# Kernel tuning notes

Hardware: AMD Instinct MI355X
Metric: run time of the kernel (lower is better)

## Reference

```python
import jax, jax.numpy as jnp
import numpy as np

MAX_VAL = 100000000.0

B, H, S, D = 4, 16, 2048, 64


def setup_inputs() -> dict:
    key = jax.random.key(0)
    kq, kk, kv, km = jax.random.split(key, 4)
    query = jax.random.normal(kq, (B, H, S, D), dtype=jnp.float32)
    key_t = jax.random.normal(kk, (B, H, S, D), dtype=jnp.float32)
    value = jax.random.normal(kv, (B, H, S, D), dtype=jnp.float32)
    mask = jax.random.randint(km, (B, 1, S, S), 0, 2, dtype=jnp.int32)
    return {"query": query, "key": key_t, "value": value, "mask": mask}


def reference(query, key, value, mask):
    d = query.shape[-1]
    # scores: [B, H, S, S]
    scores = jnp.einsum("bhqd,bhkd->bhqk", query, key) / jnp.sqrt(jnp.float32(d))
    scores = jnp.where(mask == 1, -MAX_VAL, scores)
    p_attn = jax.nn.softmax(scores, axis=-1)
    out = jnp.einsum("bhqk,bhkd->bhqd", p_attn, value)
    return out, p_attn
```

## Files before the change

kernel.cpp:

```cpp
#include <hip/hip_runtime.h>
#include <hip/hip_bf16.h>


#define SDIM 2048
#define DDIM 64
#define NB 4
#define NH 16
#define BHN 64
#define TQ 16
#define OUT_ELEMS (BHN * SDIM * DDIM)

typedef float f32x4 __attribute__((ext_vector_type(4)));
typedef __bf16 bf16x8 __attribute__((ext_vector_type(8)));
typedef __bf16 bf16x4 __attribute__((ext_vector_type(4)));
typedef __bf16 bf16;

__global__ void cvt_qk_kernel(const float* __restrict__ q, const float* __restrict__ k,
                              bf16* __restrict__ Qb, bf16* __restrict__ Kb,
                              int n8, float qscale) {
    int i = blockIdx.x * blockDim.x + threadIdx.x;
    const float* src;
    bf16* dst;
    float scale;
    if (i < n8) {
        src = q; dst = Qb; scale = qscale;
    } else {
        src = k; dst = Kb; scale = 1.0f; i -= n8;
    }
    const f32x4* s4 = (const f32x4*)src;
    f32x4 a = __builtin_nontemporal_load(s4 + 2 * i);
    f32x4 c = __builtin_nontemporal_load(s4 + 2 * i + 1);
    bf16x8 o;
    o[0] = (bf16)(a[0] * scale); o[1] = (bf16)(a[1] * scale);
    o[2] = (bf16)(a[2] * scale); o[3] = (bf16)(a[3] * scale);
    o[4] = (bf16)(c[0] * scale); o[5] = (bf16)(c[1] * scale);
    o[6] = (bf16)(c[2] * scale); o[7] = (bf16)(c[3] * scale);
    *(bf16x8*)(dst + 8 * (size_t)i) = o;
}

__global__ void transpose_v_kernel(const float* __restrict__ v, bf16* __restrict__ vt) {
    int bh = blockIdx.x >> 5;
    int k0 = (blockIdx.x & 31) * 64;
    __shared__ bf16 tile[64][72];
    int t = threadIdx.x;
    int r = t >> 4;
    int c4 = (t & 15) * 4;
    const float* vb = v + (size_t)bh * SDIM * DDIM;
#pragma unroll
    for (int i = 0; i < 4; i++) {
        int row = r + 16 * i;
        f32x4 x = __builtin_nontemporal_load(
            (const f32x4*)(vb + (size_t)(k0 + row) * DDIM + c4));
        tile[c4 + 0][row] = (bf16)x[0];
        tile[c4 + 1][row] = (bf16)x[1];
        tile[c4 + 2][row] = (bf16)x[2];
        tile[c4 + 3][row] = (bf16)x[3];
    }
    __syncthreads();
    bf16* vtb = vt + (size_t)bh * DDIM * SDIM;
    int drow = t >> 2;
    int seg = (t & 3) * 16;
    uint4 u0 = *(const uint4*)&tile[drow][seg];
    uint4 u1 = *(const uint4*)&tile[drow][seg + 8];
    *(uint4*)(vtb + (size_t)drow * SDIM + k0 + seg) = u0;
    *(uint4*)(vtb + (size_t)drow * SDIM + k0 + seg + 8) = u1;
}

__global__ void pack_mask_kernel(const int* __restrict__ src, unsigned* __restrict__ dst) {
    int i = blockIdx.x * blockDim.x + threadIdx.x;
    int mv = __builtin_nontemporal_load(src + i);
    unsigned long long bal = __ballot(mv == 1);
    int l = threadIdx.x & 63;
    if (l == 0) dst[i >> 5] = (unsigned)bal;
    else if (l == 32) dst[i >> 5] = (unsigned)(bal >> 32);
}

__launch_bounds__(256, 2)
__global__ void attn_kernel(const bf16* __restrict__ Qb, const bf16* __restrict__ Kb,
                            const bf16* __restrict__ Vtb, const unsigned* __restrict__ mbits,
                            float* __restrict__ out, float* __restrict__ p_out) {
    const int bid0 = blockIdx.x;
    const int bid = (bid0 & 7) * 1024 + (bid0 >> 3);
    const int qt = bid & 127;
    const int bh = bid >> 7;
    const int b  = bh >> 4;
    const int t = threadIdx.x;
    const int w = t >> 6;
    const int lane = t & 63;
    const int quad = lane >> 4;
    const int l15 = lane & 15;

    __shared__ bf16 pb[TQ * 2056];
    __shared__ float redmax[4][16];
    __shared__ float redsum[4][16];

    const int qrow = qt * TQ + l15;
    const bf16* qbase = Qb + ((size_t)bh * SDIM + qrow) * DDIM + 8 * quad;
    bf16x8 aq0 = *(const bf16x8*)(qbase);
    bf16x8 aq1 = *(const bf16x8*)(qbase + 32);

    const unsigned* mrow = mbits + (size_t)b * SDIM * 64
                         + (size_t)(qt * TQ + quad * 4) * 64 + w * 16;
    uint4 mw[4][4];
#pragma unroll
    for (int r = 0; r < 4; r++)
#pragma unroll
        for (int g = 0; g < 4; g++)
            mw[r][g] = *(const uint4*)(mrow + r * 64 + g * 4);

    f32x4 acc[32];
    const bf16* kbase = Kb + ((size_t)bh * SDIM + w * 512 + l15) * DDIM + 8 * quad;
#pragma unroll
    for (int kt = 0; kt < 32; kt++) {
        const bf16* kp = kbase + (size_t)kt * 16 * DDIM;
        bf16x8 b0 = *(const bf16x8*)(kp);
        bf16x8 b1 = *(const bf16x8*)(kp + 32);
        f32x4 c = {0.f, 0.f, 0.f, 0.f};
        c = __builtin_amdgcn_mfma_f32_16x16x32_bf16(aq0, b0, c, 0, 0, 0);
        c = __builtin_amdgcn_mfma_f32_16x16x32_bf16(aq1, b1, c, 0, 0, 0);
        acc[kt] = c;
    }

    const float MASKED = -1.4426950e8f;
    float mx[4] = {-3e38f, -3e38f, -3e38f, -3e38f};
#pragma unroll
    for (int kt = 0; kt < 32; kt++) {
        const int g = kt >> 3;
        const int sel = (kt >> 1) & 3;
#pragma unroll
        for (int r = 0; r < 4; r++) {
            const uint4 u = mw[r][g];
            unsigned dw = sel == 0 ? u.x : sel == 1 ? u.y : sel == 2 ? u.z : u.w;
            unsigned bits = dw >> (((kt & 1) << 4) + l15);
            float s = (bits & 1u) ? MASKED : acc[kt][r];
            acc[kt][r] = s;
            mx[r] = fmaxf(mx[r], s);
        }
    }
#pragma unroll
    for (int off = 1; off < 16; off <<= 1) {
#pragma unroll
        for (int r = 0; r < 4; r++)
            mx[r] = fmaxf(mx[r], __shfl_xor(mx[r], off, 64));
    }

    float sm[4] = {0.f, 0.f, 0.f, 0.f};
#pragma unroll
    for (int kt = 0; kt < 32; kt++) {
#pragma unroll
        for (int r = 0; r < 4; r++) {
            float e = __builtin_amdgcn_exp2f(acc[kt][r] - mx[r]);
            acc[kt][r] = e;
            sm[r] += e;
        }
    }
#pragma unroll
    for (int off = 1; off < 16; off <<= 1) {
#pragma unroll
        for (int r = 0; r < 4; r++)
            sm[r] += __shfl_xor(sm[r], off, 64);
    }

    if (l15 == 0) {
#pragma unroll
        for (int r = 0; r < 4; r++) {
            redmax[w][quad * 4 + r] = mx[r];
            redsum[w][quad * 4 + r] = sm[r];
        }
    }
    __syncthreads();
    float rs[4];
#pragma unroll
    for (int r = 0; r < 4; r++) {
        const int row = quad * 4 + r;
        float m0 = redmax[0][row], m1 = redmax[1][row];
        float m2 = redmax[2][row], m3 = redmax[3][row];
        float mg = fmaxf(fmaxf(m0, m1), fmaxf(m2, m3));
        float stot = redsum[0][row] * __builtin_amdgcn_exp2f(m0 - mg)
                   + redsum[1][row] * __builtin_amdgcn_exp2f(m1 - mg)
                   + redsum[2][row] * __builtin_amdgcn_exp2f(m2 - mg)
                   + redsum[3][row] * __builtin_amdgcn_exp2f(m3 - mg);
        rs[r] = __builtin_amdgcn_exp2f(mx[r] - mg) / stot;
    }

    const int j  = l15 & 3;
    const int c4 = l15 & 12;
    float* prow4 = p_out + (size_t)bh * SDIM * SDIM
                 + (size_t)(qt * TQ + quad * 4 + j) * SDIM + w * 512 + c4;
    bf16* pbrow = pb + (size_t)(quad * 4 + j) * 2056 + w * 512 + c4;
#pragma unroll
    for (int kt = 0; kt < 32; kt++) {
        float v0 = acc[kt][0] * rs[0];
        float v1 = acc[kt][1] * rs[1];
        float v2 = acc[kt][2] * rs[2];
        float v3 = acc[kt][3] * rs[3];
        float a  = (j & 1) ? v0 : v1;
        float bt = (j & 1) ? v2 : v3;
        a  = __shfl_xor(a, 1, 64);
        bt = __shfl_xor(bt, 1, 64);
        float nv0 = (j & 1) ? a  : v0;
        float nv1 = (j & 1) ? v1 : a;
        float nv2 = (j & 1) ? bt : v2;
        float nv3 = (j & 1) ? v3 : bt;
        a  = (j & 2) ? nv0 : nv2;
        bt = (j & 2) ? nv1 : nv3;
        a  = __shfl_xor(a, 2, 64);
        bt = __shfl_xor(bt, 2, 64);
        v0 = (j & 2) ? a   : nv0;
        v1 = (j & 2) ? bt  : nv1;
        v2 = (j & 2) ? nv2 : a;
        v3 = (j & 2) ? nv3 : bt;
        f32x4 pv = {v0, v1, v2, v3};
        __builtin_nontemporal_store(pv, (f32x4*)(prow4 + kt * 16));
        bf16x4 ph = {(bf16)v0, (bf16)v1, (bf16)v2, (bf16)v3};
        *(bf16x4*)(pbrow + kt * 16) = ph;
    }

    asm volatile("s_waitcnt lgkmcnt(0)" ::: "memory");
    __builtin_amdgcn_s_barrier();
    __builtin_amdgcn_sched_barrier(0);

    f32x4 o0 = {0.f, 0.f, 0.f, 0.f}, o1 = o0, o2 = o0, o3 = o0;
    const bf16* vbase = Vtb + ((size_t)bh * DDIM + w * 16 + l15) * SDIM + 8 * quad;
    const bf16* pbase = pb + l15 * 2056 + 8 * quad;
    __builtin_amdgcn_s_setprio(1);
#pragma unroll
    for (int ks = 0; ks < 64; ks += 4) {
        bf16x8 a0 = *(const bf16x8*)(pbase + 32 * ks);
        bf16x8 a1 = *(const bf16x8*)(pbase + 32 * (ks + 1));
        bf16x8 a2 = *(const bf16x8*)(pbase + 32 * (ks + 2));
        bf16x8 a3 = *(const bf16x8*)(pbase + 32 * (ks + 3));
        bf16x8 w0 = *(const bf16x8*)(vbase + 32 * ks);
        bf16x8 w1 = *(const bf16x8*)(vbase + 32 * (ks + 1));
        bf16x8 w2 = *(const bf16x8*)(vbase + 32 * (ks + 2));
        bf16x8 w3 = *(const bf16x8*)(vbase + 32 * (ks + 3));
        o0 = __builtin_amdgcn_mfma_f32_16x16x32_bf16(a0, w0, o0, 0, 0, 0);
        o1 = __builtin_amdgcn_mfma_f32_16x16x32_bf16(a1, w1, o1, 0, 0, 0);
        o2 = __builtin_amdgcn_mfma_f32_16x16x32_bf16(a2, w2, o2, 0, 0, 0);
        o3 = __builtin_amdgcn_mfma_f32_16x16x32_bf16(a3, w3, o3, 0, 0, 0);
    }
    __builtin_amdgcn_s_setprio(0);
    f32x4 o = (o0 + o1) + (o2 + o3);
    float* orow = out + ((size_t)bh * SDIM + qt * TQ + quad * 4) * DDIM + w * 16 + l15;
#pragma unroll
    for (int r = 0; r < 4; r++)
        __builtin_nontemporal_store(o[r], orow + (size_t)r * DDIM);
}

extern "C" void kernel_launch(void* const* d_in, const int* in_sizes, int n_in,
                              void* d_out, int out_size, void* d_ws, size_t ws_size,
                              hipStream_t stream) {
    const float* q = (const float*)d_in[0];
    const float* k = (const float*)d_in[1];
    const float* v = (const float*)d_in[2];
    const int* mask = (const int*)d_in[3];
    float* out = (float*)d_out;
    float* p = out + (size_t)OUT_ELEMS;

    bf16* Qb  = (bf16*)d_ws;
    bf16* Kb  = Qb + (size_t)BHN * SDIM * DDIM;
    bf16* Vtb = Kb + (size_t)BHN * SDIM * DDIM;
    unsigned* Mb = (unsigned*)(Vtb + (size_t)BHN * SDIM * DDIM);

    const float SC = 0.125f * 1.44269504f;
    cvt_qk_kernel<<<8192, 256, 0, stream>>>(q, k, Qb, Kb, OUT_ELEMS / 8, SC);
    transpose_v_kernel<<<BHN * (SDIM / 64), 256, 0, stream>>>(v, Vtb);
    pack_mask_kernel<<<(NB * SDIM * SDIM) / 256, 256, 0, stream>>>(mask, Mb);
    attn_kernel<<<BHN * (SDIM / TQ), 256, 0, stream>>>(Qb, Kb, Vtb, Mb, out, p);
}
```

Measured before the change: 1.599 ms.

## Split attention tile work across eight waves with LDS reduction of PV partials

Doubles the attention block to 512 threads so each wave handles 256 key columns instead of 512, halving per-thread score registers and mask words. The PV product is split into two key halves across wave pairs, and their partial outputs are combined through shared memory before storing. The aim is to raise occupancy and latency hiding on this memory-bound kernel, which writes the full P matrix. The cost is an extra barrier, more LDS, and a longer cross-wave max/sum reduction.

```diff
diff --git a/kernel.cpp b/kernel.cpp
--- a/kernel.cpp
+++ b/kernel.cpp
@@ -75,7 +75,7 @@
     else if (l == 32) dst[i >> 5] = (unsigned)(bal >> 32);
 }
 
-__launch_bounds__(256, 2)
+__launch_bounds__(512, 4)
 __global__ void attn_kernel(const bf16* __restrict__ Qb, const bf16* __restrict__ Kb,
                             const bf16* __restrict__ Vtb, const unsigned* __restrict__ mbits,
                             float* __restrict__ out, float* __restrict__ p_out) {
@@ -91,27 +91,19 @@
     const int l15 = lane & 15;
 
     __shared__ bf16 pb[TQ * 2056];
-    __shared__ float redmax[4][16];
-    __shared__ float redsum[4][16];
+    __shared__ float redmax[8][16];
+    __shared__ float redsum[8][16];
+    __shared__ f32x4 opart[4][64];
 
     const int qrow = qt * TQ + l15;
     const bf16* qbase = Qb + ((size_t)bh * SDIM + qrow) * DDIM + 8 * quad;
     bf16x8 aq0 = *(const bf16x8*)(qbase);
     bf16x8 aq1 = *(const bf16x8*)(qbase + 32);
 
-    const unsigned* mrow = mbits + (size_t)b * SDIM * 64
-                         + (size_t)(qt * TQ + quad * 4) * 64 + w * 16;
-    uint4 mw[4][4];
-#pragma unroll
-    for (int r = 0; r < 4; r++)
-#pragma unroll
-        for (int g = 0; g < 4; g++)
-            mw[r][g] = *(const uint4*)(mrow + r * 64 + g * 4);
-
-    f32x4 acc[32];
-    const bf16* kbase = Kb + ((size_t)bh * SDIM + w * 512 + l15) * DDIM + 8 * quad;
-#pragma unroll
-    for (int kt = 0; kt < 32; kt++) {
+    f32x4 acc[16];
+    const bf16* kbase = Kb + ((size_t)bh * SDIM + w * 256 + l15) * DDIM + 8 * quad;
+#pragma unroll
+    for (int kt = 0; kt < 16; kt++) {
         const bf16* kp = kbase + (size_t)kt * 16 * DDIM;
         bf16x8 b0 = *(const bf16x8*)(kp);
         bf16x8 b1 = *(const bf16x8*)(kp + 32);
@@ -121,10 +113,19 @@
         acc[kt] = c;
     }
 
+    const unsigned* mrow = mbits + (size_t)b * SDIM * 64
+                         + (size_t)(qt * TQ + quad * 4) * 64 + w * 8;
+    uint4 mw[4][2];
+#pragma unroll
+    for (int r = 0; r < 4; r++)
+#pragma unroll
+        for (int g = 0; g < 2; g++)
+            mw[r][g] = *(const uint4*)(mrow + r * 64 + g * 4);
+
     const float MASKED = -1.4426950e8f;
     float mx[4] = {-3e38f, -3e38f, -3e38f, -3e38f};
 #pragma unroll
-    for (int kt = 0; kt < 32; kt++) {
+    for (int kt = 0; kt < 16; kt++) {
         const int g = kt >> 3;
         const int sel = (kt >> 1) & 3;
 #pragma unroll
@@ -146,7 +147,7 @@
 
     float sm[4] = {0.f, 0.f, 0.f, 0.f};
 #pragma unroll
-    for (int kt = 0; kt < 32; kt++) {
+    for (int kt = 0; kt < 16; kt++) {
 #pragma unroll
         for (int r = 0; r < 4; r++) {
             float e = __builtin_amdgcn_exp2f(acc[kt][r] - mx[r]);
@@ -173,23 +174,27 @@
 #pragma unroll
     for (int r = 0; r < 4; r++) {
         const int row = quad * 4 + r;
-        float m0 = redmax[0][row], m1 = redmax[1][row];
-        float m2 = redmax[2][row], m3 = redmax[3][row];
-        float mg = fmaxf(fmaxf(m0, m1), fmaxf(m2, m3));
-        float stot = redsum[0][row] * __builtin_amdgcn_exp2f(m0 - mg)
-                   + redsum[1][row] * __builtin_amdgcn_exp2f(m1 - mg)
-                   + redsum[2][row] * __builtin_amdgcn_exp2f(m2 - mg)
-                   + redsum[3][row] * __builtin_amdgcn_exp2f(m3 - mg);
+        float mv[8];
+        float mg = -3e38f;
+#pragma unroll
+        for (int ww = 0; ww < 8; ww++) {
+            mv[ww] = redmax[ww][row];
+            mg = fmaxf(mg, mv[ww]);
+        }
+        float stot = 0.f;
+#pragma unroll
+        for (int ww = 0; ww < 8; ww++)
+            stot += redsum[ww][row] * __builtin_amdgcn_exp2f(mv[ww] - mg);
         rs[r] = __builtin_amdgcn_exp2f(mx[r] - mg) / stot;
     }
 
     const int j  = l15 & 3;
     const int c4 = l15 & 12;
     float* prow4 = p_out + (size_t)bh * SDIM * SDIM
-                 + (size_t)(qt * TQ + quad * 4 + j) * SDIM + w * 512 + c4;
-    bf16* pbrow = pb + (size_t)(quad * 4 + j) * 2056 + w * 512 + c4;
-#pragma unroll
-    for (int kt = 0; kt < 32; kt++) {
+                 + (size_t)(qt * TQ + quad * 4 + j) * SDIM + w * 256 + c4;
+    bf16* pbrow = pb + (size_t)(quad * 4 + j) * 2056 + w * 256 + c4;
+#pragma unroll
+    for (int kt = 0; kt < 16; kt++) {
         float v0 = acc[kt][0] * rs[0];
         float v1 = acc[kt][1] * rs[1];
         float v2 = acc[kt][2] * rs[2];
@@ -220,12 +225,15 @@
     __builtin_amdgcn_s_barrier();
     __builtin_amdgcn_sched_barrier(0);
 
+    const int wc = w & 3;
+    const int wh = w >> 2;
     f32x4 o0 = {0.f, 0.f, 0.f, 0.f}, o1 = o0, o2 = o0, o3 = o0;
-    const bf16* vbase = Vtb + ((size_t)bh * DDIM + w * 16 + l15) * SDIM + 8 * quad;
-    const bf16* pbase = pb + l15 * 2056 + 8 * quad;
+    const bf16* vbase = Vtb + ((size_t)bh * DDIM + wc * 16 + l15) * SDIM
+                        + 1024 * wh + 8 * quad;
+    const bf16* pbase = pb + l15 * 2056 + 1024 * wh + 8 * quad;
     __builtin_amdgcn_s_setprio(1);
 #pragma unroll
-    for (int ks = 0; ks < 64; ks += 4) {
+    for (int ks = 0; ks < 32; ks += 4) {
         bf16x8 a0 = *(const bf16x8*)(pbase + 32 * ks);
         bf16x8 a1 = *(const bf16x8*)(pbase + 32 * (ks + 1));
         bf16x8 a2 = *(const bf16x8*)(pbase + 32 * (ks + 2));
@@ -241,10 +249,18 @@
     }
     __builtin_amdgcn_s_setprio(0);
     f32x4 o = (o0 + o1) + (o2 + o3);
-    float* orow = out + ((size_t)bh * SDIM + qt * TQ + quad * 4) * DDIM + w * 16 + l15;
-#pragma unroll
-    for (int r = 0; r < 4; r++)
-        __builtin_nontemporal_store(o[r], orow + (size_t)r * DDIM);
+
+    if (w >= 4) opart[wc][lane] = o;
+    __syncthreads();
+    if (w < 4) {
+        f32x4 op = opart[wc][lane];
+        f32x4 oo = o + op;
+        float* orow = out + ((size_t)bh * SDIM + qt * TQ + quad * 4) * DDIM
+                      + wc * 16 + l15;
+#pragma unroll
+        for (int r = 0; r < 4; r++)
+            __builtin_nontemporal_store(oo[r], orow + (size_t)r * DDIM);
+    }
 }
 
 extern "C" void kernel_launch(void* const* d_in, const int* in_sizes, int n_in,
@@ -266,5 +282,5 @@
     cvt_qk_kernel<<<8192, 256, 0, stream>>>(q, k, Qb, Kb, OUT_ELEMS / 8, SC);
     transpose_v_kernel<<<BHN * (SDIM / 64), 256, 0, stream>>>(v, Vtb);
     pack_mask_kernel<<<(NB * SDIM * SDIM) / 256, 256, 0, stream>>>(mask, Mb);
-    attn_kernel<<<BHN * (SDIM / TQ), 256, 0, stream>>>(Qb, Kb, Vtb, Mb, out, p);
-}
+    attn_kernel<<<BHN * (SDIM / TQ), 512, 0, stream>>>(Qb, Kb, Vtb, Mb, out, p);
+}
```

Result: slower. 1.633 ms (+2.1%).
